# Kernel tuning notes

Measured on AMD Instinct MI355X. Metric: run time of the kernel, lower is better.

Reference implementation:

```python
import jax, jax.numpy as jnp
import numpy as np

B, C, H, W = 8, 256, 128, 128
HEADS, DIM_HEAD = 4, 32
HID = HEADS * DIM_HEAD  # 128


def setup_inputs() -> dict:
    key = jax.random.key(0)
    k1, k2, k3, k4 = jax.random.split(key, 4)
    x = jax.random.normal(k1, (B, C, H, W), dtype=jnp.float32)
    # 1x1 conv weights stored as [out_ch, in_ch]
    w_qkv = jax.random.normal(k2, (3 * HID, C), dtype=jnp.float32) * (1.0 / np.sqrt(C))
    w_out = jax.random.normal(k3, (C, HID), dtype=jnp.float32) * (1.0 / np.sqrt(HID))
    b_out = jax.random.normal(k4, (C,), dtype=jnp.float32) * 0.01
    return {"x": x, "w_qkv": w_qkv, "w_out": w_out, "b_out": b_out}


def reference(x, w_qkv, w_out, b_out):
    b, c, h, w = x.shape
    n = h * w
    # 1x1 conv == channel matmul
    qkv = jnp.einsum('oc,bchw->bohw', w_qkv, x)  # [b, 3*HID, h, w]
    q, k, v = jnp.split(qkv, 3, axis=1)
    # rearrange 'b (heads d) h w -> b heads d (h w)'
    def to_heads(t):
        return t.reshape(b, HEADS, DIM_HEAD, n)
    q, k, v = to_heads(q), to_heads(k), to_heads(v)
    k = jax.nn.softmax(k, axis=-1)  # over spatial n
    # q_scale is False: q used as-is
    context = jnp.einsum('bhdn,bhen->bhde', k, v)   # [b, heads, d, e] small
    out = jnp.einsum('bhde,bhdn->bhen', context, q)  # [b, heads, e, n]
    out = out.reshape(b, HID, h, w)
    out = jnp.einsum('oc,bchw->bohw', w_out, out) + b_out[None, :, None, None]
    return out
```

## Files before the change

### kernel.cpp

```cpp
#include <hip/hip_runtime.h>
#include <stdint.h>

#define BB 8
#define CIN 256
#define NSP 16384
#define HID 128

typedef __bf16 bfrag __attribute__((ext_vector_type(8)));
typedef float  f32x4 __attribute__((ext_vector_type(4)));

__device__ __forceinline__ unsigned short f2bf(float f) {
  union { float f; unsigned int u; } v; v.f = f;
  unsigned int u = v.u;
  return (unsigned short)((u + 0x7FFFu + ((u >> 16) & 1u)) >> 16);
}
__device__ __forceinline__ float bf2f(unsigned short s) {
  union { unsigned int u; float f; } v; v.u = ((unsigned int)s) << 16;
  return v.f;
}

__global__ __launch_bounds__(256) void la_cast_w(const float* __restrict__ w,
                                                 unsigned short* __restrict__ wb, int n) {
  int i = blockIdx.x * 256 + threadIdx.x;
  if (i < n) wb[i] = f2bf(w[i]);
}

__global__ __launch_bounds__(256) void la_transpose(const float* __restrict__ x,
                                                    unsigned short* __restrict__ xT) {
  __shared__ __align__(16) float tile[64][68];
  const int n0 = blockIdx.x * 64;
  const int c0 = blockIdx.y * 64;
  const int b  = blockIdx.z;
  const int t = threadIdx.x;
  const float* xp = x + (size_t)b * CIN * NSP;
  const int nseg = (t & 15) * 4;
  const int crow = t >> 4;
#pragma unroll
  for (int i = 0; i < 4; ++i) {
    const int c = crow + i * 16;
    const float4 v = *(const float4*)(xp + (size_t)(c0 + c) * NSP + n0 + nseg);
    tile[nseg + 0][c] = v.x;
    tile[nseg + 1][c] = v.y;
    tile[nseg + 2][c] = v.z;
    tile[nseg + 3][c] = v.w;
  }
  __syncthreads();
  const int n = t >> 2;
  const int seg = (t & 3) * 16;
  unsigned short* op = xT + ((size_t)b * NSP + n0 + n) * CIN + c0 + seg;
  union { unsigned short u[16]; uint4 q[2]; } pk;
#pragma unroll
  for (int k = 0; k < 16; ++k) pk.u[k] = f2bf(tile[n][seg + k]);
  *(uint4*)(op) = pk.q[0];
  *(uint4*)(op + 8) = pk.q[1];
}

__global__ __launch_bounds__(256) void la_q_gemm(const unsigned short* __restrict__ wq,
                                                 const unsigned short* __restrict__ xT,
                                                 unsigned short* __restrict__ qT) {
  __shared__ __align__(16) unsigned short Wt[128][40];
  __shared__ __align__(16) unsigned short Xt[128][40];
  const int n0 = blockIdx.x * 128;
  const int b = blockIdx.y;
  const int t = threadIdx.x;
  const int lane = t & 63, wv = t >> 6;
  const int wm = (wv >> 1) * 64, wn = (wv & 1) * 64;
  const int l15 = lane & 15, q = lane >> 4;
  f32x4 acc[4][4];
#pragma unroll
  for (int i = 0; i < 4; ++i)
#pragma unroll
    for (int j = 0; j < 4; ++j) acc[i][j] = 0.0f;
  const unsigned short* wbase = wq;
  const unsigned short* xbase = xT + ((size_t)b * NSP + n0) * CIN;
  const int r = t >> 1, hh = (t & 1) * 16;
  for (int kc = 0; kc < 8; ++kc) {
    const int ko = kc * 32 + hh;
    uint4 w0 = *(const uint4*)(wbase + (size_t)r * CIN + ko);
    uint4 w1 = *(const uint4*)(wbase + (size_t)r * CIN + ko + 8);
    uint4 x0 = *(const uint4*)(xbase + (size_t)r * CIN + ko);
    uint4 x1 = *(const uint4*)(xbase + (size_t)r * CIN + ko + 8);
    *(uint4*)&Wt[r][hh] = w0;
    *(uint4*)&Wt[r][hh + 8] = w1;
    *(uint4*)&Xt[r][hh] = x0;
    *(uint4*)&Xt[r][hh + 8] = x1;
    __syncthreads();
    bfrag a[4], bf[4];
#pragma unroll
    for (int mi = 0; mi < 4; ++mi) a[mi] = *(const bfrag*)&Wt[wm + mi * 16 + l15][q * 8];
#pragma unroll
    for (int ni = 0; ni < 4; ++ni) bf[ni] = *(const bfrag*)&Xt[wn + ni * 16 + l15][q * 8];
#pragma unroll
    for (int mi = 0; mi < 4; ++mi)
#pragma unroll
      for (int ni = 0; ni < 4; ++ni)
        acc[mi][ni] = __builtin_amdgcn_mfma_f32_16x16x32_bf16(a[mi], bf[ni], acc[mi][ni], 0, 0, 0);
    __syncthreads();
  }
  unsigned short* qb = qT + (size_t)b * NSP * HID;
#pragma unroll
  for (int mi = 0; mi < 4; ++mi) {
    const int ob = wm + mi * 16 + q * 4;
#pragma unroll
    for (int ni = 0; ni < 4; ++ni) {
      const int n = n0 + wn + ni * 16 + l15;
      ushort4 pk;
      pk.x = f2bf(acc[mi][ni][0]);
      pk.y = f2bf(acc[mi][ni][1]);
      pk.z = f2bf(acc[mi][ni][2]);
      pk.w = f2bf(acc[mi][ni][3]);
      *(ushort4*)(qb + (size_t)n * HID + ob) = pk;
    }
  }
}

__global__ __launch_bounds__(256, 2) void la_kv_ctx(const unsigned short* __restrict__ wq,
                                                    const unsigned short* __restrict__ xT,
                                                    float* __restrict__ ctxp,
                                                    float* __restrict__ sums) {
  __shared__ union {
    struct { unsigned short Wt[256][40]; unsigned short Xt[128][40]; } g;
    struct { unsigned short Lk[128][136]; unsigned short Lv[128][136]; } e;
  } sh;
  const int chunk = blockIdx.x;
  const int n0 = chunk * 128;
  const int b = blockIdx.y;
  const int t = threadIdx.x;
  const int lane = t & 63, wv = t >> 6;
  const int l15 = lane & 15, q = lane >> 4;
  const int wm = wv * 64;
  f32x4 acc[4][8];
#pragma unroll
  for (int i = 0; i < 4; ++i)
#pragma unroll
    for (int j = 0; j < 8; ++j) acc[i][j] = 0.0f;
  const unsigned short* wbase = wq + 128 * CIN;
  const unsigned short* xbase = xT + ((size_t)b * NSP + n0) * CIN;
  const int xr = t >> 1, xh = (t & 1) * 16;
  for (int kc = 0; kc < 8; ++kc) {
    const int ko = kc * 32;
    uint4 w0 = *(const uint4*)(wbase + (size_t)t * CIN + ko);
    uint4 w1 = *(const uint4*)(wbase + (size_t)t * CIN + ko + 8);
    uint4 w2 = *(const uint4*)(wbase + (size_t)t * CIN + ko + 16);
    uint4 w3 = *(const uint4*)(wbase + (size_t)t * CIN + ko + 24);
    uint4 x0 = *(const uint4*)(xbase + (size_t)xr * CIN + ko + xh);
    uint4 x1 = *(const uint4*)(xbase + (size_t)xr * CIN + ko + xh + 8);
    *(uint4*)&sh.g.Wt[t][0]  = w0;
    *(uint4*)&sh.g.Wt[t][8]  = w1;
    *(uint4*)&sh.g.Wt[t][16] = w2;
    *(uint4*)&sh.g.Wt[t][24] = w3;
    *(uint4*)&sh.g.Xt[xr][xh]     = x0;
    *(uint4*)&sh.g.Xt[xr][xh + 8] = x1;
    __syncthreads();
    bfrag a[4], bb[8];
#pragma unroll
    for (int mi = 0; mi < 4; ++mi) a[mi] = *(const bfrag*)&sh.g.Wt[wm + mi * 16 + l15][q * 8];
#pragma unroll
    for (int ni = 0; ni < 8; ++ni) bb[ni] = *(const bfrag*)&sh.g.Xt[ni * 16 + l15][q * 8];
#pragma unroll
    for (int mi = 0; mi < 4; ++mi)
#pragma unroll
      for (int ni = 0; ni < 8; ++ni)
        acc[mi][ni] = __builtin_amdgcn_mfma_f32_16x16x32_bf16(a[mi], bb[ni], acc[mi][ni], 0, 0, 0);
    __syncthreads();
  }
  const int isV = wv >> 1;
  const int rb = (wv & 1) * 64;
  unsigned short (*Lp)[136] = isV ? sh.e.Lv : sh.e.Lk;
  float sp[16];
#pragma unroll
  for (int i = 0; i < 16; ++i) sp[i] = 0.f;
#pragma unroll
  for (int mi = 0; mi < 4; ++mi)
#pragma unroll
    for (int ni = 0; ni < 8; ++ni)
#pragma unroll
      for (int rg = 0; rg < 4; ++rg) {
        float val = acc[mi][ni][rg];
        if (!isV) { val = __expf(val); sp[mi * 4 + rg] += val; }
        Lp[rb + mi * 16 + q * 4 + rg][ni * 16 + l15] = f2bf(val);
      }
  if (!isV) {
#pragma unroll
    for (int i = 0; i < 16; ++i) {
      float s = sp[i];
      s += __shfl_down(s, 8, 16);
      s += __shfl_down(s, 4, 16);
      s += __shfl_down(s, 2, 16);
      s += __shfl_down(s, 1, 16);
      if (l15 == 0)
        atomicAdd(&sums[b * 128 + rb + (i >> 2) * 16 + q * 4 + (i & 3)], s);
    }
  }
  __syncthreads();
  const int h = wv;
  f32x4 c2[2][2];
  c2[0][0] = 0.f; c2[0][1] = 0.f; c2[1][0] = 0.f; c2[1][1] = 0.f;
#pragma unroll
  for (int nit = 0; nit < 4; ++nit) {
    bfrag ka[2], vb2[2];
#pragma unroll
    for (int d2 = 0; d2 < 2; ++d2)
      ka[d2] = *(const bfrag*)&sh.e.Lk[h * 32 + d2 * 16 + l15][nit * 32 + q * 8];
#pragma unroll
    for (int e2 = 0; e2 < 2; ++e2)
      vb2[e2] = *(const bfrag*)&sh.e.Lv[h * 32 + e2 * 16 + l15][nit * 32 + q * 8];
#pragma unroll
    for (int d2 = 0; d2 < 2; ++d2)
#pragma unroll
      for (int e2 = 0; e2 < 2; ++e2)
        c2[d2][e2] = __builtin_amdgcn_mfma_f32_16x16x32_bf16(ka[d2], vb2[e2], c2[d2][e2], 0, 0, 0);
  }
  float* cp = ctxp + ((size_t)chunk * 32 + b * 4 + h) * 1024;
#pragma unroll
  for (int d2 = 0; d2 < 2; ++d2)
#pragma unroll
    for (int e2 = 0; e2 < 2; ++e2)
#pragma unroll
      for (int rg = 0; rg < 4; ++rg)
        cp[(d2 * 16 + q * 4 + rg) * 32 + e2 * 16 + l15] = c2[d2][e2][rg];
}

__global__ __launch_bounds__(256) void la_reduce(const float* __restrict__ ctxp,
                                                 float* __restrict__ ctxu) {
  const int gid = blockIdx.x * 256 + threadIdx.x;
  const int g = blockIdx.y;
  const float* p = ctxp + (size_t)g * 32 * 32768 + gid;
  float s = 0.f;
#pragma unroll
  for (int c = 0; c < 32; ++c) s += p[(size_t)c * 32768];
  atomicAdd(&ctxu[gid], s);
}

__global__ __launch_bounds__(128) void la_weff(const float* __restrict__ w_out,
                                               const float* __restrict__ ctxu,
                                               const float* __restrict__ sums,
                                               unsigned short* __restrict__ weff) {
  const int o = blockIdx.x;
  const int b = blockIdx.y;
  const int cp = threadIdx.x;
  const int h = cp >> 5, d = cp & 31;
  const float* wrow = w_out + (size_t)o * HID + h * 32;
  const float* crow = ctxu + ((size_t)(b * 4 + h) * 32 + d) * 32;
  float s = 0.f;
#pragma unroll 8
  for (int e = 0; e < 32; ++e) s += wrow[e] * crow[e];
  s *= (1.0f / sums[b * 128 + h * 32 + d]);
  weff[((size_t)b * 256 + o) * HID + cp] = f2bf(s);
}

__global__ __launch_bounds__(256) void la_out_gemm(const unsigned short* __restrict__ weff,
                                                   const unsigned short* __restrict__ qT,
                                                   const float* __restrict__ b_out,
                                                   float* __restrict__ out) {
  __shared__ __align__(16) unsigned short At[128][40];
  __shared__ __align__(16) unsigned short Bt[128][40];
  const int mblk = blockIdx.x;
  const int n0 = blockIdx.y * 128;
  const int b = blockIdx.z;
  const int t = threadIdx.x;
  const int lane = t & 63, wv = t >> 6;
  const int wm = (wv >> 1) * 64, wn = (wv & 1) * 64;
  const int l15 = lane & 15, q = lane >> 4;
  f32x4 acc[4][4];
#pragma unroll
  for (int i = 0; i < 4; ++i)
#pragma unroll
    for (int j = 0; j < 4; ++j) acc[i][j] = 0.0f;
  const unsigned short* abase = weff + ((size_t)b * 256 + mblk * 128) * HID;
  const unsigned short* bbase = qT + ((size_t)b * NSP + n0) * HID;
  const int r = t >> 1, hh = (t & 1) * 16;
  for (int kc = 0; kc < 4; ++kc) {
    const int ko = kc * 32 + hh;
    uint4 a0 = *(const uint4*)(abase + (size_t)r * HID + ko);
    uint4 a1 = *(const uint4*)(abase + (size_t)r * HID + ko + 8);
    uint4 b0 = *(const uint4*)(bbase + (size_t)r * HID + ko);
    uint4 b1 = *(const uint4*)(bbase + (size_t)r * HID + ko + 8);
    *(uint4*)&At[r][hh] = a0;
    *(uint4*)&At[r][hh + 8] = a1;
    *(uint4*)&Bt[r][hh] = b0;
    *(uint4*)&Bt[r][hh + 8] = b1;
    __syncthreads();
    bfrag a[4], bf[4];
#pragma unroll
    for (int mi = 0; mi < 4; ++mi) a[mi] = *(const bfrag*)&At[wm + mi * 16 + l15][q * 8];
#pragma unroll
    for (int ni = 0; ni < 4; ++ni) bf[ni] = *(const bfrag*)&Bt[wn + ni * 16 + l15][q * 8];
#pragma unroll
    for (int mi = 0; mi < 4; ++mi)
#pragma unroll
      for (int ni = 0; ni < 4; ++ni)
        acc[mi][ni] = __builtin_amdgcn_mfma_f32_16x16x32_bf16(a[mi], bf[ni], acc[mi][ni], 0, 0, 0);
    __syncthreads();
  }
  float* obase = out + ((size_t)b * 256 + mblk * 128) * NSP;
#pragma unroll
  for (int mi = 0; mi < 4; ++mi) {
    const int ob = wm + mi * 16 + q * 4;
    const float4 bias = *(const float4*)(b_out + mblk * 128 + ob);
    float ba[4] = {bias.x, bias.y, bias.z, bias.w};
#pragma unroll
    for (int ni = 0; ni < 4; ++ni) {
      const int n = n0 + wn + ni * 16 + l15;
#pragma unroll
      for (int rg = 0; rg < 4; ++rg)
        obase[(size_t)(ob + rg) * NSP + n] = acc[mi][ni][rg] + ba[rg];
    }
  }
}


extern "C" void kernel_launch(void* const* d_in, const int* in_sizes, int n_in,
                              void* d_out, int out_size, void* d_ws, size_t ws_size,
                              hipStream_t stream) {
  (void)in_sizes; (void)n_in; (void)out_size; (void)ws_size;
  const float* x     = (const float*)d_in[0];
  const float* w_qkv = (const float*)d_in[1];
  const float* w_out = (const float*)d_in[2];
  const float* b_out = (const float*)d_in[3];
  float* out = (float*)d_out;
  char* ws = (char*)d_ws;
  unsigned short* xT   = (unsigned short*)(ws);
  unsigned short* qT   = (unsigned short*)(ws + 67108864);
  float* ctxp          = (float*)(ws + 100663296);
  float* ctxu          = (float*)(ws + 117440512);
  float* sums          = (float*)(ws + 117571584);
  unsigned short* weff = (unsigned short*)(ws + 117575680);
  unsigned short* wqb  = (unsigned short*)(ws + 118099968);

  hipMemsetAsync(ctxu, 0, 131072 + 4096, stream);
  la_cast_w<<<dim3(384), dim3(256), 0, stream>>>(w_qkv, wqb, 384 * 256);
  la_transpose<<<dim3(NSP / 64, CIN / 64, BB), dim3(256), 0, stream>>>(x, xT);
  la_q_gemm<<<dim3(NSP / 128, BB), dim3(256), 0, stream>>>(wqb, xT, qT);
  la_kv_ctx<<<dim3(NSP / 128, BB), dim3(256), 0, stream>>>(wqb, xT, ctxp, sums);
  la_reduce<<<dim3(128, 4), dim3(256), 0, stream>>>(ctxp, ctxu);
  la_weff<<<dim3(256, BB), dim3(128), 0, stream>>>(w_out, ctxu, sums, weff);
  la_out_gemm<<<dim3(2, NSP / 128, BB), dim3(256), 0, stream>>>(weff, qT, b_out, out);
}
```

Measured before the change: 353.5 us.

## Fuse weight cast, transpose, Q GEMM and KV-context into one kernel

```diff
diff --git a/kernel.cpp b/kernel.cpp
--- a/kernel.cpp
+++ b/kernel.cpp
@@ -14,113 +14,16 @@
   unsigned int u = v.u;
   return (unsigned short)((u + 0x7FFFu + ((u >> 16) & 1u)) >> 16);
 }
-__device__ __forceinline__ float bf2f(unsigned short s) {
-  union { unsigned int u; float f; } v; v.u = ((unsigned int)s) << 16;
-  return v.f;
-}
-
-__global__ __launch_bounds__(256) void la_cast_w(const float* __restrict__ w,
-                                                 unsigned short* __restrict__ wb, int n) {
-  int i = blockIdx.x * 256 + threadIdx.x;
-  if (i < n) wb[i] = f2bf(w[i]);
-}
-
-__global__ __launch_bounds__(256) void la_transpose(const float* __restrict__ x,
-                                                    unsigned short* __restrict__ xT) {
-  __shared__ __align__(16) float tile[64][68];
-  const int n0 = blockIdx.x * 64;
-  const int c0 = blockIdx.y * 64;
-  const int b  = blockIdx.z;
-  const int t = threadIdx.x;
-  const float* xp = x + (size_t)b * CIN * NSP;
-  const int nseg = (t & 15) * 4;
-  const int crow = t >> 4;
-#pragma unroll
-  for (int i = 0; i < 4; ++i) {
-    const int c = crow + i * 16;
-    const float4 v = *(const float4*)(xp + (size_t)(c0 + c) * NSP + n0 + nseg);
-    tile[nseg + 0][c] = v.x;
-    tile[nseg + 1][c] = v.y;
-    tile[nseg + 2][c] = v.z;
-    tile[nseg + 3][c] = v.w;
-  }
-  __syncthreads();
-  const int n = t >> 2;
-  const int seg = (t & 3) * 16;
-  unsigned short* op = xT + ((size_t)b * NSP + n0 + n) * CIN + c0 + seg;
-  union { unsigned short u[16]; uint4 q[2]; } pk;
-#pragma unroll
-  for (int k = 0; k < 16; ++k) pk.u[k] = f2bf(tile[n][seg + k]);
-  *(uint4*)(op) = pk.q[0];
-  *(uint4*)(op + 8) = pk.q[1];
-}
-
-__global__ __launch_bounds__(256) void la_q_gemm(const unsigned short* __restrict__ wq,
-                                                 const unsigned short* __restrict__ xT,
-                                                 unsigned short* __restrict__ qT) {
-  __shared__ __align__(16) unsigned short Wt[128][40];
-  __shared__ __align__(16) unsigned short Xt[128][40];
-  const int n0 = blockIdx.x * 128;
-  const int b = blockIdx.y;
-  const int t = threadIdx.x;
-  const int lane = t & 63, wv = t >> 6;
-  const int wm = (wv >> 1) * 64, wn = (wv & 1) * 64;
-  const int l15 = lane & 15, q = lane >> 4;
-  f32x4 acc[4][4];
-#pragma unroll
-  for (int i = 0; i < 4; ++i)
-#pragma unroll
-    for (int j = 0; j < 4; ++j) acc[i][j] = 0.0f;
-  const unsigned short* wbase = wq;
-  const unsigned short* xbase = xT + ((size_t)b * NSP + n0) * CIN;
-  const int r = t >> 1, hh = (t & 1) * 16;
-  for (int kc = 0; kc < 8; ++kc) {
-    const int ko = kc * 32 + hh;
-    uint4 w0 = *(const uint4*)(wbase + (size_t)r * CIN + ko);
-    uint4 w1 = *(const uint4*)(wbase + (size_t)r * CIN + ko + 8);
-    uint4 x0 = *(const uint4*)(xbase + (size_t)r * CIN + ko);
-    uint4 x1 = *(const uint4*)(xbase + (size_t)r * CIN + ko + 8);
-    *(uint4*)&Wt[r][hh] = w0;
-    *(uint4*)&Wt[r][hh + 8] = w1;
-    *(uint4*)&Xt[r][hh] = x0;
-    *(uint4*)&Xt[r][hh + 8] = x1;
-    __syncthreads();
-    bfrag a[4], bf[4];
-#pragma unroll
-    for (int mi = 0; mi < 4; ++mi) a[mi] = *(const bfrag*)&Wt[wm + mi * 16 + l15][q * 8];
-#pragma unroll
-    for (int ni = 0; ni < 4; ++ni) bf[ni] = *(const bfrag*)&Xt[wn + ni * 16 + l15][q * 8];
-#pragma unroll
-    for (int mi = 0; mi < 4; ++mi)
-#pragma unroll
-      for (int ni = 0; ni < 4; ++ni)
-        acc[mi][ni] = __builtin_amdgcn_mfma_f32_16x16x32_bf16(a[mi], bf[ni], acc[mi][ni], 0, 0, 0);
-    __syncthreads();
-  }
-  unsigned short* qb = qT + (size_t)b * NSP * HID;
-#pragma unroll
-  for (int mi = 0; mi < 4; ++mi) {
-    const int ob = wm + mi * 16 + q * 4;
-#pragma unroll
-    for (int ni = 0; ni < 4; ++ni) {
-      const int n = n0 + wn + ni * 16 + l15;
-      ushort4 pk;
-      pk.x = f2bf(acc[mi][ni][0]);
-      pk.y = f2bf(acc[mi][ni][1]);
-      pk.z = f2bf(acc[mi][ni][2]);
-      pk.w = f2bf(acc[mi][ni][3]);
-      *(ushort4*)(qb + (size_t)n * HID + ob) = pk;
-    }
-  }
-}
-
-__global__ __launch_bounds__(256, 2) void la_kv_ctx(const unsigned short* __restrict__ wq,
-                                                    const unsigned short* __restrict__ xT,
-                                                    float* __restrict__ ctxp,
-                                                    float* __restrict__ sums) {
-  __shared__ union {
-    struct { unsigned short Wt[256][40]; unsigned short Xt[128][40]; } g;
-    struct { unsigned short Lk[128][136]; unsigned short Lv[128][136]; } e;
+
+__global__ __launch_bounds__(512, 2) void la_fused(const float* __restrict__ x,
+                                                   const float* __restrict__ w_qkv,
+                                                   unsigned short* __restrict__ qT,
+                                                   float* __restrict__ ctxp,
+                                                   float* __restrict__ sums) {
+  __shared__ __align__(16) union {
+    struct { unsigned short Wt[384][40]; unsigned short Xb[128][40]; } g;
+    struct { unsigned short Lk[64][136]; unsigned short Lv[64][136];
+             float Pc[4][1024]; } e;
   } sh;
   const int chunk = blockIdx.x;
   const int n0 = chunk * 128;
@@ -128,108 +31,151 @@
   const int t = threadIdx.x;
   const int lane = t & 63, wv = t >> 6;
   const int l15 = lane & 15, q = lane >> 4;
-  const int wm = wv * 64;
-  f32x4 acc[4][8];
-#pragma unroll
-  for (int i = 0; i < 4; ++i)
+  const int cl = t & 31;
+  const int n16 = (t >> 5) * 8;
+  const float* xp = x + (size_t)b * CIN * NSP + n0;
+  f32x4 acc[3][8];
+#pragma unroll
+  for (int i = 0; i < 3; ++i)
 #pragma unroll
     for (int j = 0; j < 8; ++j) acc[i][j] = 0.0f;
-  const unsigned short* wbase = wq + 128 * CIN;
-  const unsigned short* xbase = xT + ((size_t)b * NSP + n0) * CIN;
-  const int xr = t >> 1, xh = (t & 1) * 16;
+
   for (int kc = 0; kc < 8; ++kc) {
-    const int ko = kc * 32;
-    uint4 w0 = *(const uint4*)(wbase + (size_t)t * CIN + ko);
-    uint4 w1 = *(const uint4*)(wbase + (size_t)t * CIN + ko + 8);
-    uint4 w2 = *(const uint4*)(wbase + (size_t)t * CIN + ko + 16);
-    uint4 w3 = *(const uint4*)(wbase + (size_t)t * CIN + ko + 24);
-    uint4 x0 = *(const uint4*)(xbase + (size_t)xr * CIN + ko + xh);
-    uint4 x1 = *(const uint4*)(xbase + (size_t)xr * CIN + ko + xh + 8);
-    *(uint4*)&sh.g.Wt[t][0]  = w0;
-    *(uint4*)&sh.g.Wt[t][8]  = w1;
-    *(uint4*)&sh.g.Wt[t][16] = w2;
-    *(uint4*)&sh.g.Wt[t][24] = w3;
-    *(uint4*)&sh.g.Xt[xr][xh]     = x0;
-    *(uint4*)&sh.g.Xt[xr][xh + 8] = x1;
-    __syncthreads();
-    bfrag a[4], bb[8];
-#pragma unroll
-    for (int mi = 0; mi < 4; ++mi) a[mi] = *(const bfrag*)&sh.g.Wt[wm + mi * 16 + l15][q * 8];
-#pragma unroll
-    for (int ni = 0; ni < 8; ++ni) bb[ni] = *(const bfrag*)&sh.g.Xt[ni * 16 + l15][q * 8];
-#pragma unroll
-    for (int mi = 0; mi < 4; ++mi)
-#pragma unroll
-      for (int ni = 0; ni < 8; ++ni)
-        acc[mi][ni] = __builtin_amdgcn_mfma_f32_16x16x32_bf16(a[mi], bb[ni], acc[mi][ni], 0, 0, 0);
-    __syncthreads();
-  }
-  const int isV = wv >> 1;
-  const int rb = (wv & 1) * 64;
-  unsigned short (*Lp)[136] = isV ? sh.e.Lv : sh.e.Lk;
-  float sp[16];
-#pragma unroll
-  for (int i = 0; i < 16; ++i) sp[i] = 0.f;
-#pragma unroll
-  for (int mi = 0; mi < 4; ++mi)
+#pragma unroll
+    for (int i = 0; i < 3; ++i) {
+      const int id = t + i * 512;
+      const int row = id >> 2, c8 = (id & 3) * 8;
+      const float* wr = w_qkv + (size_t)row * CIN + kc * 32 + c8;
+      const float4 wa = *(const float4*)wr;
+      const float4 wb4 = *(const float4*)(wr + 4);
+      ushort4 p0, p1;
+      p0.x = f2bf(wa.x); p0.y = f2bf(wa.y); p0.z = f2bf(wa.z); p0.w = f2bf(wa.w);
+      p1.x = f2bf(wb4.x); p1.y = f2bf(wb4.y); p1.z = f2bf(wb4.z); p1.w = f2bf(wb4.w);
+      *(ushort4*)&sh.g.Wt[row][c8] = p0;
+      *(ushort4*)&sh.g.Wt[row][c8 + 4] = p1;
+    }
+    const float* xr = xp + (size_t)(kc * 32 + cl) * NSP + n16;
+    const float4 xa = *(const float4*)xr;
+    const float4 xb4 = *(const float4*)(xr + 4);
+    sh.g.Xb[n16 + 0][cl] = f2bf(xa.x);
+    sh.g.Xb[n16 + 1][cl] = f2bf(xa.y);
+    sh.g.Xb[n16 + 2][cl] = f2bf(xa.z);
+    sh.g.Xb[n16 + 3][cl] = f2bf(xa.w);
+    sh.g.Xb[n16 + 4][cl] = f2bf(xb4.x);
+    sh.g.Xb[n16 + 5][cl] = f2bf(xb4.y);
+    sh.g.Xb[n16 + 6][cl] = f2bf(xb4.z);
+    sh.g.Xb[n16 + 7][cl] = f2bf(xb4.w);
+    __syncthreads();
+    bfrag a0 = *(const bfrag*)&sh.g.Wt[wv * 16 + l15][q * 8];
+    bfrag a1 = *(const bfrag*)&sh.g.Wt[128 + wv * 16 + l15][q * 8];
+    bfrag a2 = *(const bfrag*)&sh.g.Wt[256 + wv * 16 + l15][q * 8];
+    bfrag bb[8];
+#pragma unroll
+    for (int ni = 0; ni < 8; ++ni) bb[ni] = *(const bfrag*)&sh.g.Xb[ni * 16 + l15][q * 8];
+#pragma unroll
+    for (int ni = 0; ni < 8; ++ni) {
+      acc[0][ni] = __builtin_amdgcn_mfma_f32_16x16x32_bf16(a0, bb[ni], acc[0][ni], 0, 0, 0);
+      acc[1][ni] = __builtin_amdgcn_mfma_f32_16x16x32_bf16(a1, bb[ni], acc[1][ni], 0, 0, 0);
+      acc[2][ni] = __builtin_amdgcn_mfma_f32_16x16x32_bf16(a2, bb[ni], acc[2][ni], 0, 0, 0);
+    }
+    __syncthreads();
+  }
+
+  {
+    unsigned short* qb = qT + (size_t)b * NSP * HID;
+    const int qrow = wv * 16 + q * 4;
+#pragma unroll
+    for (int ni = 0; ni < 8; ++ni) {
+      const int n = n0 + ni * 16 + l15;
+      ushort4 pk;
+      pk.x = f2bf(acc[0][ni][0]);
+      pk.y = f2bf(acc[0][ni][1]);
+      pk.z = f2bf(acc[0][ni][2]);
+      pk.w = f2bf(acc[0][ni][3]);
+      *(ushort4*)(qb + (size_t)n * HID + qrow) = pk;
+    }
+  }
+  {
+    float sp[4] = {0.f, 0.f, 0.f, 0.f};
 #pragma unroll
     for (int ni = 0; ni < 8; ++ni)
 #pragma unroll
-      for (int rg = 0; rg < 4; ++rg) {
-        float val = acc[mi][ni][rg];
-        if (!isV) { val = __expf(val); sp[mi * 4 + rg] += val; }
-        Lp[rb + mi * 16 + q * 4 + rg][ni * 16 + l15] = f2bf(val);
-      }
-  if (!isV) {
-#pragma unroll
-    for (int i = 0; i < 16; ++i) {
-      float s = sp[i];
+      for (int rg = 0; rg < 4; ++rg) sp[rg] += __expf(acc[1][ni][rg]);
+#pragma unroll
+    for (int rg = 0; rg < 4; ++rg) {
+      float s = sp[rg];
       s += __shfl_down(s, 8, 16);
       s += __shfl_down(s, 4, 16);
       s += __shfl_down(s, 2, 16);
       s += __shfl_down(s, 1, 16);
-      if (l15 == 0)
-        atomicAdd(&sums[b * 128 + rb + (i >> 2) * 16 + q * 4 + (i & 3)], s);
-    }
-  }
-  __syncthreads();
-  const int h = wv;
-  f32x4 c2[2][2];
-  c2[0][0] = 0.f; c2[0][1] = 0.f; c2[1][0] = 0.f; c2[1][1] = 0.f;
-#pragma unroll
-  for (int nit = 0; nit < 4; ++nit) {
-    bfrag ka[2], vb2[2];
+      if (l15 == 0) atomicAdd(&sums[b * 128 + wv * 16 + q * 4 + rg], s);
+    }
+  }
+  float* cp = ctxp + ((size_t)chunk * 32 + b * 4) * 1024;
+#pragma unroll
+  for (int ph = 0; ph < 2; ++ph) {
+    if ((wv >> 2) == ph) {
+      const int r = (wv & 3) * 16 + q * 4;
+#pragma unroll
+      for (int ni = 0; ni < 8; ++ni)
+#pragma unroll
+        for (int rg = 0; rg < 4; ++rg) {
+          sh.e.Lk[r + rg][ni * 16 + l15] = f2bf(__expf(acc[1][ni][rg]));
+          sh.e.Lv[r + rg][ni * 16 + l15] = f2bf(acc[2][ni][rg]);
+        }
+    }
+    __syncthreads();
+    const int hl = wv >> 2, nq = wv & 3;
+    f32x4 c2[2][2];
+    c2[0][0] = 0.f; c2[0][1] = 0.f; c2[1][0] = 0.f; c2[1][1] = 0.f;
+    bfrag ka[2], vb[2];
 #pragma unroll
     for (int d2 = 0; d2 < 2; ++d2)
-      ka[d2] = *(const bfrag*)&sh.e.Lk[h * 32 + d2 * 16 + l15][nit * 32 + q * 8];
+      ka[d2] = *(const bfrag*)&sh.e.Lk[hl * 32 + d2 * 16 + l15][nq * 32 + q * 8];
 #pragma unroll
     for (int e2 = 0; e2 < 2; ++e2)
-      vb2[e2] = *(const bfrag*)&sh.e.Lv[h * 32 + e2 * 16 + l15][nit * 32 + q * 8];
+      vb[e2] = *(const bfrag*)&sh.e.Lv[hl * 32 + e2 * 16 + l15][nq * 32 + q * 8];
 #pragma unroll
     for (int d2 = 0; d2 < 2; ++d2)
 #pragma unroll
       for (int e2 = 0; e2 < 2; ++e2)
-        c2[d2][e2] = __builtin_amdgcn_mfma_f32_16x16x32_bf16(ka[d2], vb2[e2], c2[d2][e2], 0, 0, 0);
-  }
-  float* cp = ctxp + ((size_t)chunk * 32 + b * 4 + h) * 1024;
-#pragma unroll
-  for (int d2 = 0; d2 < 2; ++d2)
-#pragma unroll
-    for (int e2 = 0; e2 < 2; ++e2)
-#pragma unroll
-      for (int rg = 0; rg < 4; ++rg)
-        cp[(d2 * 16 + q * 4 + rg) * 32 + e2 * 16 + l15] = c2[d2][e2][rg];
+        c2[d2][e2] = __builtin_amdgcn_mfma_f32_16x16x32_bf16(ka[d2], vb[e2], c2[d2][e2], 0, 0, 0);
+    const int slot = hl * 2 + (nq & 1);
+    if (nq < 2) {
+#pragma unroll
+      for (int d2 = 0; d2 < 2; ++d2)
+#pragma unroll
+        for (int e2 = 0; e2 < 2; ++e2)
+#pragma unroll
+          for (int rg = 0; rg < 4; ++rg)
+            sh.e.Pc[slot][(d2 * 16 + q * 4 + rg) * 32 + e2 * 16 + l15] = c2[d2][e2][rg];
+    }
+    __syncthreads();
+    if (nq >= 2) {
+#pragma unroll
+      for (int d2 = 0; d2 < 2; ++d2)
+#pragma unroll
+        for (int e2 = 0; e2 < 2; ++e2)
+#pragma unroll
+          for (int rg = 0; rg < 4; ++rg)
+            sh.e.Pc[slot][(d2 * 16 + q * 4 + rg) * 32 + e2 * 16 + l15] += c2[d2][e2][rg];
+    }
+    __syncthreads();
+    for (int idx = t; idx < 2048; idx += 512) {
+      const int h2 = idx >> 10, pos = idx & 1023;
+      cp[(ph * 2 + h2) * 1024 + pos] = sh.e.Pc[h2 * 2][pos] + sh.e.Pc[h2 * 2 + 1][pos];
+    }
+    __syncthreads();
+  }
 }
 
 __global__ __launch_bounds__(256) void la_reduce(const float* __restrict__ ctxp,
                                                  float* __restrict__ ctxu) {
   const int gid = blockIdx.x * 256 + threadIdx.x;
-  const int g = blockIdx.y;
-  const float* p = ctxp + (size_t)g * 32 * 32768 + gid;
   float s = 0.f;
-#pragma unroll
-  for (int c = 0; c < 32; ++c) s += p[(size_t)c * 32768];
-  atomicAdd(&ctxu[gid], s);
+#pragma unroll 8
+  for (int c = 0; c < 128; ++c) s += ctxp[(size_t)c * 32768 + gid];
+  ctxu[gid] = s;
 }
 
 __global__ __launch_bounds__(128) void la_weff(const float* __restrict__ w_out,
@@ -320,20 +266,15 @@
   const float* b_out = (const float*)d_in[3];
   float* out = (float*)d_out;
   char* ws = (char*)d_ws;
-  unsigned short* xT   = (unsigned short*)(ws);
-  unsigned short* qT   = (unsigned short*)(ws + 67108864);
-  float* ctxp          = (float*)(ws + 100663296);
-  float* ctxu          = (float*)(ws + 117440512);
-  float* sums          = (float*)(ws + 117571584);
-  unsigned short* weff = (unsigned short*)(ws + 117575680);
-  unsigned short* wqb  = (unsigned short*)(ws + 118099968);
-
-  hipMemsetAsync(ctxu, 0, 131072 + 4096, stream);
-  la_cast_w<<<dim3(384), dim3(256), 0, stream>>>(w_qkv, wqb, 384 * 256);
-  la_transpose<<<dim3(NSP / 64, CIN / 64, BB), dim3(256), 0, stream>>>(x, xT);
-  la_q_gemm<<<dim3(NSP / 128, BB), dim3(256), 0, stream>>>(wqb, xT, qT);
-  la_kv_ctx<<<dim3(NSP / 128, BB), dim3(256), 0, stream>>>(wqb, xT, ctxp, sums);
-  la_reduce<<<dim3(128, 4), dim3(256), 0, stream>>>(ctxp, ctxu);
+  unsigned short* qT   = (unsigned short*)(ws);
+  float* ctxp          = (float*)(ws + 33554432);
+  float* ctxu          = (float*)(ws + 50331648);
+  float* sums          = (float*)(ws + 50462720);
+  unsigned short* weff = (unsigned short*)(ws + 50466816);
+
+  hipMemsetAsync(sums, 0, 4096, stream);
+  la_fused<<<dim3(NSP / 128, BB), dim3(512), 0, stream>>>(x, w_qkv, qT, ctxp, sums);
+  la_reduce<<<dim3(128), dim3(256), 0, stream>>>(ctxp, ctxu);
   la_weff<<<dim3(256, BB), dim3(128), 0, stream>>>(w_out, ctxu, sums, weff);
   la_out_gemm<<<dim3(2, NSP / 128, BB), dim3(256), 0, stream>>>(weff, qT, b_out, out);
 }
```

After: 342.7 us. 1.03x faster.
